# Kernel optimization log

Hardware: AMD Instinct MI355X
Metric: run time of the kernel (lower is better)

The kernel has to match this reference:

```python
import jax, jax.numpy as jnp
import numpy as np

BASE_RES = 192          # image_shape = [192, 192]
VIEWS = 128             # radial views
READOUT_OS = 2.0        # readout oversampling
SAMPLES = int(BASE_RES * READOUT_OS)  # 384 samples per spoke


def _radial_traj_and_weights():
    """Linear-ordered full-range 2D radial trajectory + ramp density weights."""
    t = jnp.arange(SAMPLES, dtype=jnp.float32)
    # radius spans [-pi, pi) along each spoke (NUFFT convention)
    r = (t - SAMPLES / 2) / (SAMPLES / 2) * jnp.pi            # [samples]
    theta = jnp.arange(VIEWS, dtype=jnp.float32) * (jnp.pi / VIEWS)  # [views]
    kx = r[None, :] * jnp.cos(theta)[:, None]                 # [views, samples]
    ky = r[None, :] * jnp.sin(theta)[:, None]
    points = jnp.stack([kx, ky], axis=-1).reshape(-1, 2)      # [M, 2]
    # geometric (ramp) density compensation: weight ~ |k| with DC floor
    rho = jnp.abs(r) / jnp.pi                                 # [samples], in [0, 1]
    w = jnp.maximum(rho, 1.0 / SAMPLES)                       # avoid zero at DC
    weights = jnp.broadcast_to(w[None, :], (VIEWS, SAMPLES)).reshape(-1)  # [M]
    return points, weights


def setup_inputs() -> dict:
    key = jax.random.key(0)
    x = jax.random.normal(key, (2, BASE_RES, BASE_RES, 2), dtype=jnp.float32)
    points, weights = _radial_traj_and_weights()
    return {"x": x, "points": points, "weights": weights}


def _nudft_resample(xc, points, weights):
    """Type-2 NUDFT (forward) -> density comp -> type-1 NUDFT (adjoint).

    xc: complex [C, B, H, W]; points: [M, 2] in [-pi, pi); weights: [M].
    The 2D nonuniform DFT phase factorizes per axis: exp(-i(kx*nx + ky*ny)).
    """
    C, B, H, W = xc.shape
    nx = (jnp.arange(H, dtype=jnp.float32) - H // 2)          # grid indices
    ny = (jnp.arange(W, dtype=jnp.float32) - W // 2)
    Ax = jnp.exp(-1j * (points[:, 0:1] * nx[None, :]).astype(jnp.complex64))  # [M, H]
    Ay = jnp.exp(-1j * (points[:, 1:2] * ny[None, :]).astype(jnp.complex64))  # [M, W]
    # type-2: k[m] = sum_{h,w} x[h,w] exp(-i(kx_m h + ky_m w))
    tmp = jnp.einsum('cbhw,mh->cbmw', xc, Ax)                 # [C, B, M, W]
    k = jnp.einsum('cbmw,mw->cbm', tmp, Ay)                   # [C, B, M]
    # density compensation
    k = k * weights.astype(jnp.complex64)
    # type-1 adjoint: img[h,w] = sum_m k[m] exp(+i(kx_m h + ky_m w))
    tmp2 = jnp.einsum('cbm,mh->cbmh', k, jnp.conj(Ax))        # [C, B, M, H]
    img = jnp.einsum('cbmh,mw->cbhw', tmp2, jnp.conj(Ay))     # [C, B, H, W]
    # scale by 1 / num_elements(image_shape)
    return img / jnp.asarray(H * W, dtype=jnp.complex64)


def reference(x, points, weights):
    # inputs [B, H, W, C] -> channels-first [C, B, H, W] (layer's perm)
    rank = x.ndim
    perm = [rank - 1] + list(range(rank - 1))
    xc = jnp.transpose(x, perm).astype(jnp.complex64)
    img = _nudft_resample(xc, points, weights)
    out = jnp.abs(img)                                        # layer dtype is real
    inv_perm = list(range(1, rank)) + [0]
    return jnp.transpose(out, inv_perm)                       # [B, H, W, C]
```

## Files before the change

kernel.cpp:

```cpp
#include <hip/hip_runtime.h>
#include <math.h>


#define HH 192
#define WW 192
#define NVIEWS 128
#define NSAMP 384
#define NPIX (HH*WW)
#define HALFT 193
#define M2 12545
#define M2P 12672
#define KTOT 25344
#define NSPLITK 33

typedef __attribute__((ext_vector_type(8))) short bf16x8;
typedef __attribute__((ext_vector_type(4))) float f32x4;
typedef __attribute__((ext_vector_type(8))) unsigned short u16x8;

__device__ __forceinline__ void rot(float& cr, float& ci, float dr, float di) {
  float nr = cr*dr - ci*di;
  float ni = cr*di + ci*dr;
  cr = nr; ci = ni;
}
__device__ __forceinline__ unsigned short f2b(float f) {
  unsigned int u = __float_as_uint(f);
  u += 0x7fffu + ((u >> 16) & 1u);
  return (unsigned short)(u >> 16);
}
__device__ __forceinline__ float b2f(unsigned short h) {
  return __uint_as_float(((unsigned int)h) << 16);
}

__global__ __launch_bounds__(256) void phase_kernel(
    const float* __restrict__ points, const float* __restrict__ x,
    unsigned short* __restrict__ BT, unsigned short* __restrict__ CxT,
    unsigned short* __restrict__ SxT, unsigned short* __restrict__ Am,
    unsigned short* __restrict__ XT, float* __restrict__ kyv) {
  const int v2 = blockIdx.x;
  const int role = blockIdx.y;
  const int t = threadIdx.x;
  if (role == 24) {
    for (int idx = v2*256 + t; idx < 768*192; idx += 65*256) {
      const int n = idx / 192, h = idx - n*192;
      const int cb = n / 192, w = n - cb*192;
      const int b = cb >> 1, c = cb & 1;
      XT[idx] = f2b(x[(((size_t)b*HH + h)*WW + w)*2 + c]);
    }
    for (int idx = v2*256 + t; idx < M2P; idx += 65*256) {
      if (idx < M2) {
        const int v2b = idx / HALFT, tb = idx - v2b*HALFT;
        kyv[idx] = points[(v2b*NSAMP + tb)*2 + 1];
      } else {
        kyv[idx] = 0.f;
      }
    }
    return;
  }
  if (t >= HALFT) return;
  if (role < 12) {
    const int hsplit = role;
    const float kx = points[(v2*NSAMP + t)*2 + 0];
    const int m2 = v2*HALFT + t;
    const int h0 = hsplit*16;
    float cr, ci; __sincosf(kx*(float)(h0-96), &ci, &cr);
    float dr, di; __sincosf(kx, &di, &dr);
    u16x8 pc, ps;
    #pragma unroll
    for (int j = 0; j < 16; ++j) {
      const int h = h0 + j;
      CxT[(size_t)h*M2P + m2] = f2b(cr);
      SxT[(size_t)h*M2P + m2] = f2b(ci);
      pc[j&7] = f2b(cr); ps[j&7] = f2b(ci);
      if ((j&7) == 7) {
        *(u16x8*)(Am + (size_t)m2*192 + (h-7))         = pc;
        *(u16x8*)(Am + (size_t)(12672+m2)*192 + (h-7)) = ps;
      }
      rot(cr, ci, dr, di);
    }
  } else {
    const int wsplit = role - 12;
    const float ky = points[(v2*NSAMP + t)*2 + 1];
    const int kap = v2*HALFT + t;
    const int w0 = wsplit*16;
    float cr, ci; __sincosf(ky*(float)(w0-96), &ci, &cr);
    float dr, di; __sincosf(ky, &di, &dr);
    #pragma unroll
    for (int j = 0; j < 16; ++j) {
      BT[(size_t)(w0+j)*KTOT + kap]       = f2b(cr);
      BT[(size_t)(w0+j)*KTOT + M2P + kap] = f2b(ci);
      rot(cr, ci, dr, di);
    }
  }
}


__global__ __launch_bounds__(256) void gemm1_kernel(
    const unsigned short* __restrict__ Am, const unsigned short* __restrict__ XT,
    const float* __restrict__ kyv, float* __restrict__ Abuf) {
  __shared__ float lds[2][128][2];
  const int L = blockIdx.x;
  const int idx0 = (L & 7)*99 + (L >> 3);
  const int mt = idx0 >> 2;
  const int cb = idx0 & 3;
  const int wv = threadIdx.x >> 6;
  const int lane = threadIdx.x & 63;
  const int r = lane & 15, kg = lane >> 4;
  const int mhalf = wv >> 1;
  const int whalf = wv & 1;
  const int mbase = mt*128 + mhalf*64;
  const int wbase = whalf*96;
  const int nbase = cb*192 + wbase;

  f32x4 acc[4][6];
  #pragma unroll
  for (int a = 0; a < 4; ++a)
    #pragma unroll
    for (int b = 0; b < 6; ++b) acc[a][b] = (f32x4){0.f,0.f,0.f,0.f};

  const unsigned short* Ap = Am + (size_t)(mbase + r)*192 + kg*8;
  const unsigned short* Bp = XT + (size_t)(nbase + r)*192 + kg*8;
  #pragma unroll
  for (int ks = 0; ks < 6; ++ks) {
    bf16x8 af[4], bfr[6];
    #pragma unroll
    for (int mf = 0; mf < 4; ++mf)
      af[mf] = *(const bf16x8*)(Ap + (size_t)mf*16*192 + ks*32);
    #pragma unroll
    for (int nf = 0; nf < 6; ++nf)
      bfr[nf] = *(const bf16x8*)(Bp + (size_t)nf*16*192 + ks*32);
    #pragma unroll
    for (int mf = 0; mf < 4; ++mf)
      #pragma unroll
      for (int nf = 0; nf < 6; ++nf)
        acc[mf][nf] = __builtin_amdgcn_mfma_f32_16x16x32_bf16(
            af[mf], bfr[nf], acc[mf][nf], 0, 0, 0);
  }

  const bool isCx = (mt < 99);
  const int m2w = mbase - (isCx ? 0 : 12672);
  float accA[16], accB[16];
  #pragma unroll
  for (int mf = 0; mf < 4; ++mf)
    #pragma unroll
    for (int reg = 0; reg < 4; ++reg) {
      const int m2 = m2w + mf*16 + kg*4 + reg;
      const float ky = kyv[m2];
      float sy, cy; __sincosf(ky*(float)(wbase + r - 96), &sy, &cy);
      float ds, dc; __sincosf(ky*16.0f, &ds, &dc);
      float a0 = 0.f, b0 = 0.f;
      #pragma unroll
      for (int nf = 0; nf < 6; ++nf) {
        const float g = acc[mf][nf][reg];
        a0 = fmaf(g, cy, a0);
        b0 = fmaf(g, sy, b0);
        rot(cy, sy, dc, ds);
      }
      accA[mf*4+reg] = a0; accB[mf*4+reg] = b0;
    }
  #pragma unroll
  for (int msk = 1; msk <= 8; msk <<= 1) {
    #pragma unroll
    for (int i = 0; i < 16; ++i) {
      accA[i] += __shfl_xor(accA[i], msk);
      accB[i] += __shfl_xor(accB[i], msk);
    }
  }
  if (r == 0) {
    #pragma unroll
    for (int mf = 0; mf < 4; ++mf)
      #pragma unroll
      for (int reg = 0; reg < 4; ++reg) {
        const int mloc = mhalf*64 + mf*16 + kg*4 + reg;
        lds[whalf][mloc][0] = accA[mf*4+reg];
        lds[whalf][mloc][1] = accB[mf*4+reg];
      }
  }
  __syncthreads();
  {
    const int tid = threadIdx.x;
    const int mloc = tid >> 1, slot = tid & 1;
    const float val = lds[0][mloc][slot] + lds[1][mloc][slot];
    const int m2 = mt*128 + mloc - (isCx ? 0 : 12672);
    const int oidx = isCx ? (slot ? 3 : 0) : (slot ? 1 : 2);
    Abuf[((size_t)cb*M2P + m2)*4 + oidx] = val;
  }
}


__global__ __launch_bounds__(256) void tmat_kernel(
    const float* __restrict__ Abuf, const float* __restrict__ weights,
    const unsigned short* __restrict__ CxT, const unsigned short* __restrict__ SxT,
    unsigned short* __restrict__ A, float* __restrict__ K2edge) {
  const int m2 = blockIdx.x*256 + threadIdx.x;
  if (m2 >= M2P) return;
  const int role = blockIdx.y;
  if (role == 192) {
    if (m2 >= M2) return;
    const int v2 = m2 / HALFT, t = m2 - v2*HALFT;
    if (t != 0 && t != 192) return;
    const float f = weights[t] * (1.0f/36864.0f);
    const bool hp = (v2 >= 1 && v2 <= 63);
    const int d = (t == 0) ? 0 : 1;
    #pragma unroll
    for (int cb = 0; cb < 4; ++cb) {
      const float4 Av = *(const float4*)(Abuf + ((size_t)cb*M2P + m2)*4);
      const float A1 = Av.x, A2 = Av.y, A3 = Av.z, A4 = Av.w;
      float* e = K2edge + ((v2*2 + d)*4 + cb)*2;
      e[0] = f*(A1 - A2); e[1] = -f*(A3 + A4);
      if (hp) {
        float* e2 = K2edge + (((128 - v2)*2 + d)*4 + cb)*2;
        e2[0] = f*(A1 + A2); e2[1] = f*(A3 - A4);
      }
    }
    return;
  }
  const int h = role;
  if (m2 >= M2) {
    #pragma unroll
    for (int cb = 0; cb < 4; ++cb) {
      unsigned short* Arow = A + (size_t)(cb*192 + h)*KTOT;
      Arow[m2] = 0; Arow[M2P + m2] = 0;
    }
    return;
  }
  const int v2 = m2 / HALFT, t = m2 - v2*HALFT;
  float f = weights[t] * (1.0f/36864.0f);
  if (t != 0 && t != 192) f *= 2.0f;
  const bool hp = (v2 >= 1 && v2 <= 63);
  const float cx = b2f(CxT[(size_t)h*M2P + m2]);
  const float sx = b2f(SxT[(size_t)h*M2P + m2]);
  #pragma unroll
  for (int cb = 0; cb < 4; ++cb) {
    const float4 Av = *(const float4*)(Abuf + ((size_t)cb*M2P + m2)*4);
    const float A1 = Av.x, A2 = Av.y, A3 = Av.z, A4 = Av.w;
    float p0, p1, q0, q1;
    if (hp) {
      p0 = 2.f*f*A1; p1 = 2.f*f*A3; q0 = 2.f*f*A4; q1 = 2.f*f*A2;
    } else {
      const float kr = f*(A1 - A2), ki = -f*(A3 + A4);
      p0 = kr; p1 = -ki; q0 = -ki; q1 = -kr;
    }
    unsigned short* Arow = A + (size_t)(cb*192 + h)*KTOT;
    Arow[m2]       = f2b(p0*cx + p1*sx);
    Arow[M2P + m2] = f2b(q0*cx + q1*sx);
  }
}

__global__ __launch_bounds__(256) void adj_gemm(
    const unsigned short* __restrict__ A, const unsigned short* __restrict__ BT,
    float* __restrict__ partials) {
  const int L = blockIdx.x;
  const int xcd = L & 7, slot = L >> 3;
  const int g = slot / 6;
  const int kc = g*8 + xcd;
  if (kc >= NSPLITK) return;
  const int mt = slot - g*6;
  const int wv = threadIdx.x >> 6;
  const int lane = threadIdx.x & 63;
  const int r = lane & 15, kg = lane >> 4;
  const int jbase = mt*128 + (wv>>1)*64;
  const int wbase = (wv&1)*96;
  const int kb = kc*768 + kg*8;

  f32x4 acc[4][6];
  #pragma unroll
  for (int a = 0; a < 4; ++a)
    #pragma unroll
    for (int b = 0; b < 6; ++b) acc[a][b] = (f32x4){0.f,0.f,0.f,0.f};

  const unsigned short* Ap = A + (size_t)(jbase + r)*KTOT + kb;
  const unsigned short* Bp = BT + (size_t)(wbase + r)*KTOT + kb;
  for (int ks = 0; ks < 24; ++ks) {
    bf16x8 af[4], bfr[6];
    #pragma unroll
    for (int mf = 0; mf < 4; ++mf)
      af[mf] = *(const bf16x8*)(Ap + (size_t)mf*16*KTOT + ks*32);
    #pragma unroll
    for (int nf = 0; nf < 6; ++nf)
      bfr[nf] = *(const bf16x8*)(Bp + (size_t)nf*16*KTOT + ks*32);
    #pragma unroll
    for (int mf = 0; mf < 4; ++mf)
      #pragma unroll
      for (int nf = 0; nf < 6; ++nf)
        acc[mf][nf] = __builtin_amdgcn_mfma_f32_16x16x32_bf16(
            af[mf], bfr[nf], acc[mf][nf], 0, 0, 0);
  }
  float* base = partials + (size_t)kc*192*768;
  #pragma unroll
  for (int mf = 0; mf < 4; ++mf)
    #pragma unroll
    for (int nf = 0; nf < 6; ++nf) {
      const int w = wbase + nf*16 + r;
      const int j = jbase + mf*16 + kg*4;
      *(f32x4*)(base + (size_t)w*768 + j) = acc[mf][nf];
    }
}

__global__ __launch_bounds__(256) void finish_kernel(
    const unsigned short* __restrict__ BT, const unsigned short* __restrict__ CxT,
    const unsigned short* __restrict__ SxT, const float* __restrict__ K2edge,
    const float* __restrict__ partials, float* __restrict__ out) {
  __shared__ float cxs[65][8], sxs[65][8], cys[65][8], sys[65][8];
  __shared__ float redI[4][64][4], redR[4][64][4];
  const int bx = blockIdx.x;
  const int h0 = (bx/24)*8, w0 = (bx%24)*8;
  const int tid = threadIdx.x;
  for (int i = tid; i < 65*8; i += 256) {
    const int v2 = i >> 3, e = i & 7;
    const int kap = v2*HALFT;
    cxs[v2][e] = b2f(CxT[(size_t)(h0+e)*M2P + kap]);
    sxs[v2][e] = b2f(SxT[(size_t)(h0+e)*M2P + kap]);
    cys[v2][e] = b2f(BT[(size_t)(w0+e)*KTOT + kap]);
    sys[v2][e] = b2f(BT[(size_t)(w0+e)*KTOT + M2P + kap]);
  }
  __syncthreads();
  const int g = tid >> 6, hi = (tid >> 3) & 7, wi = tid & 7;
  const int h = h0 + hi, w = w0 + wi;
  float im[4] = {0,0,0,0};
  for (int v = g*32; v < g*32 + 32; ++v) {
    const int v2 = (v <= 64) ? v : 128 - v;
    const float sg = (v <= 64) ? 1.f : -1.f;
    const float cx = cxs[v2][hi], sx = sg*sxs[v2][hi];
    const float cy = cys[v2][wi], sy = sys[v2][wi];
    const float t1 = cx*sy + sx*cy;
    const float t2 = cx*cy - sx*sy;
    const int idx = v*16;
    #pragma unroll
    for (int cb = 0; cb < 4; ++cb)
      im[cb] += K2edge[idx + cb*2]*t1 + K2edge[idx + cb*2 + 1]*t2;
  }
  float re[4] = {0,0,0,0};
  for (int kc = g; kc < NSPLITK; kc += 4) {
    const float* p = partials + (size_t)kc*147456 + (size_t)w*768;
    #pragma unroll
    for (int cb = 0; cb < 4; ++cb)
      re[cb] += p[cb*192 + h];
  }
  const int p = tid & 63;
  #pragma unroll
  for (int cb = 0; cb < 4; ++cb) { redI[g][p][cb] = im[cb]; redR[g][p][cb] = re[cb]; }
  __syncthreads();
  if (g == 0) {
    #pragma unroll
    for (int cb = 0; cb < 4; ++cb) {
      im[cb] += redI[1][p][cb] + redI[2][p][cb] + redI[3][p][cb];
      re[cb] += redR[1][p][cb] + redR[2][p][cb] + redR[3][p][cb];
    }
    const int pix = h*192 + w;
    #pragma unroll
    for (int b = 0; b < 2; ++b)
      #pragma unroll
      for (int c = 0; c < 2; ++c) {
        const int cb = b*2 + c;
        out[((size_t)b*NPIX + pix)*2 + c] = sqrtf(re[cb]*re[cb] + im[cb]*im[cb]);
      }
  }
}


template <int HPER>
__global__ __launch_bounds__(192) void fwd_kernel(
    const float* __restrict__ x, const float* __restrict__ points,
    float* __restrict__ kpart) {
  const int v = blockIdx.x;
  const int split = blockIdx.y;
  const int t = threadIdx.x;
  const int m = v*NSAMP + t;
  const float kx = points[2*m+0];
  const float ky = points[2*m+1];
  const int h0 = split*HPER;

  float kr[4] = {0,0,0,0}, ki[4] = {0,0,0,0};
  float cyr, cyi; __sincosf(96.0f*ky, &cyi, &cyr);
  float dyr, dyi; __sincosf(-ky, &dyi, &dyr);
  float cx0r, cx0i; __sincosf(kx*(float)(96-h0), &cx0i, &cx0r);
  float dxr, dxi; __sincosf(-kx, &dxi, &dxr);

  for (int wp = 0; wp < 96; ++wp) {
    const int w0 = wp*2;
    float g0r[4]={0,0,0,0}, g0i[4]={0,0,0,0};
    float g1r[4]={0,0,0,0}, g1i[4]={0,0,0,0};
    float cxr = cx0r, cxi = cx0i;
    const float* p0 = x + (h0*WW + w0)*2;
    const float* p1 = p0 + HH*WW*2;
    #pragma unroll 4
    for (int h = 0; h < HPER; ++h) {
      float4 a = *(const float4*)(p0 + h*(WW*2));
      float4 b = *(const float4*)(p1 + h*(WW*2));
      g0r[0] += a.x*cxr; g0i[0] += a.x*cxi;
      g0r[1] += a.y*cxr; g0i[1] += a.y*cxi;
      g1r[0] += a.z*cxr; g1i[0] += a.z*cxi;
      g1r[1] += a.w*cxr; g1i[1] += a.w*cxi;
      g0r[2] += b.x*cxr; g0i[2] += b.x*cxi;
      g0r[3] += b.y*cxr; g0i[3] += b.y*cxi;
      g1r[2] += b.z*cxr; g1i[2] += b.z*cxi;
      g1r[3] += b.w*cxr; g1i[3] += b.w*cxi;
      rot(cxr, cxi, dxr, dxi);
    }
    #pragma unroll
    for (int cb = 0; cb < 4; ++cb) {
      kr[cb] += g0r[cb]*cyr - g0i[cb]*cyi;
      ki[cb] += g0r[cb]*cyi + g0i[cb]*cyr;
    }
    rot(cyr, cyi, dyr, dyi);
    #pragma unroll
    for (int cb = 0; cb < 4; ++cb) {
      kr[cb] += g1r[cb]*cyr - g1i[cb]*cyi;
      ki[cb] += g1r[cb]*cyi + g1i[cb]*cyr;
    }
    rot(cyr, cyi, dyr, dyi);
  }
  float* o = kpart + (((split*NVIEWS + v)*192 + t)*4)*2;
  #pragma unroll
  for (int cb = 0; cb < 4; ++cb) { o[2*cb] = kr[cb]; o[2*cb+1] = ki[cb]; }
}

__global__ __launch_bounds__(256) void dc_kernel(
    const float* __restrict__ x, float* __restrict__ dcsum) {
  const int tid = threadIdx.x;
  float s0=0.f, s1=0.f, s2=0.f, s3=0.f;
  for (int i = tid; i < NPIX; i += 256) {
    float2 a = *(const float2*)(x + i*2);
    float2 b = *(const float2*)(x + HH*WW*2 + i*2);
    s0 += a.x; s1 += a.y; s2 += b.x; s3 += b.y;
  }
  #pragma unroll
  for (int off = 32; off > 0; off >>= 1) {
    s0 += __shfl_down(s0, off);
    s1 += __shfl_down(s1, off);
    s2 += __shfl_down(s2, off);
    s3 += __shfl_down(s3, off);
  }
  __shared__ float red[4][4];
  const int wv = tid >> 6, ln = tid & 63;
  if (ln == 0) { red[0][wv]=s0; red[1][wv]=s1; red[2][wv]=s2; red[3][wv]=s3; }
  __syncthreads();
  if (tid < 4) {
    float tot = red[tid][0]+red[tid][1]+red[tid][2]+red[tid][3];
    dcsum[2*tid] = tot; dcsum[2*tid+1] = 0.0f;
  }
}

__global__ __launch_bounds__(256) void combine_kernel(
    const float* __restrict__ kpart, const float* __restrict__ dcsum,
    const float* __restrict__ weights, float* __restrict__ K2, int nsplit) {
  const int idx = blockIdx.x*256 + threadIdx.x;
  if (idx >= NVIEWS*HALFT) return;
  const int v = idx / HALFT, t = idx % HALFT;
  float f = weights[t] * (1.0f/36864.0f);
  if (t != 0 && t != 192) f *= 2.0f;
  float o[8];
  if (t == 192) {
    #pragma unroll
    for (int cb = 0; cb < 4; ++cb) { o[2*cb] = f*dcsum[2*cb]; o[2*cb+1] = f*dcsum[2*cb+1]; }
  } else {
    #pragma unroll
    for (int cb = 0; cb < 4; ++cb) {
      float ar = 0.f, ai = 0.f;
      for (int s = 0; s < nsplit; ++s) {
        const float* p = kpart + (((s*NVIEWS + v)*192 + t)*4 + cb)*2;
        ar += p[0]; ai += p[1];
      }
      o[2*cb] = f*ar; o[2*cb+1] = f*ai;
    }
  }
  float* q = K2 + idx*8;
  #pragma unroll
  for (int j = 0; j < 8; ++j) q[j] = o[j];
}

template <int VPC>
__global__ __launch_bounds__(256) void adj_kernel(
    const float* __restrict__ K2, const float* __restrict__ points,
    float* __restrict__ imgpart) {
  const int pix = blockIdx.x*256 + threadIdx.x;
  const int chunk = blockIdx.y;
  const float nh = (float)(pix / WW - 96);
  const float nw = (float)(pix % WW - 96);
  float re[4] = {0,0,0,0}, im[4] = {0,0,0,0};
  const float INVPI = 0.3183098861837907f;
  const float PI192 = 3.14159265358979f / 192.0f;
  for (int v = chunk*VPC; v < chunk*VPC + VPC; ++v) {
    const float ct = -points[2*(v*NSAMP)+0] * INVPI;
    const float st = -points[2*(v*NSAMP)+1] * INVPI;
    const float alpha = ct*nh + st*nw;
    const float delta = alpha * PI192;
    float dr, di; __sincosf(delta, &di, &dr);
    float c0r, c0i; __sincosf(-192.0f*delta, &c0i, &c0r);
    const float* Kv = K2 + v*HALFT*8;
    #pragma unroll
    for (int cb = 0; cb < 4; ++cb) {
      float a = Kv[2*cb], b = Kv[2*cb+1];
      re[cb] += a*c0r - b*c0i;
      im[cb] += a*c0i + b*c0r;
    }
    float d2r = dr*dr - di*di, d2i = 2.0f*dr*di;
    float ar = c0r*dr - c0i*di, ai = c0r*di + c0i*dr;
    float br = ar*dr - ai*di,  bi = ar*di + ai*dr;
    for (int i = 0; i < 95; ++i) {
      const float* ka = Kv + (2*i+1)*8;
      const float* kb = Kv + (2*i+2)*8;
      #pragma unroll
      for (int cb = 0; cb < 4; ++cb)
        re[cb] += ka[2*cb]*ar - ka[2*cb+1]*ai;
      #pragma unroll
      for (int cb = 0; cb < 4; ++cb)
        re[cb] += kb[2*cb]*br - kb[2*cb+1]*bi;
      rot(ar, ai, d2r, d2i);
      rot(br, bi, d2r, d2i);
    }
    {
      const float* ka = Kv + 191*8;
      #pragma unroll
      for (int cb = 0; cb < 4; ++cb)
        re[cb] += ka[2*cb]*ar - ka[2*cb+1]*ai;
    }
    const float* kd = Kv + 192*8;
    #pragma unroll
    for (int cb = 0; cb < 4; ++cb) { re[cb] += kd[2*cb]; im[cb] += kd[2*cb+1]; }
  }
  float* o = imgpart + (chunk*NPIX + pix)*8;
  #pragma unroll
  for (int cb = 0; cb < 4; ++cb) { o[2*cb] = re[cb]; o[2*cb+1] = im[cb]; }
}

__global__ __launch_bounds__(256) void out_fb_kernel(
    const float* __restrict__ imgpart, float* __restrict__ out, int nchunk) {
  const int pix = blockIdx.x*256 + threadIdx.x;
  float re[4] = {0,0,0,0}, im[4] = {0,0,0,0};
  for (int ch = 0; ch < nchunk; ++ch) {
    const float* p = imgpart + (ch*NPIX + pix)*8;
    #pragma unroll
    for (int cb = 0; cb < 4; ++cb) { re[cb] += p[2*cb]; im[cb] += p[2*cb+1]; }
  }
  #pragma unroll
  for (int b = 0; b < 2; ++b)
    #pragma unroll
    for (int c = 0; c < 2; ++c) {
      const int cb = b*2 + c;
      out[(b*NPIX + pix)*2 + c] = sqrtf(re[cb]*re[cb] + im[cb]*im[cb]);
    }
}

extern "C" void kernel_launch(void* const* d_in, const int* in_sizes, int n_in,
                              void* d_out, int out_size, void* d_ws, size_t ws_size,
                              hipStream_t stream) {
  const float* x       = (const float*)d_in[0];
  const float* points  = (const float*)d_in[1];
  const float* weights = (const float*)d_in[2];
  float* out = (float*)d_out;

  const size_t OFF_S   = 20334080ull;
  const size_t SZ_AADJ = 38928384ull;
  const size_t NEED    = OFF_S + SZ_AADJ + 33ull*589824;

  if (ws_size >= NEED) {
    char* wsb = (char*)d_ws;
    unsigned short* BT   = (unsigned short*)(wsb + 0);
    unsigned short* CxT  = (unsigned short*)(wsb + 9732096);
    unsigned short* SxT  = (unsigned short*)(wsb + 14598144);
    float* K2edge        = (float*)(wsb + 19464192);
    float* kyv           = (float*)(wsb + 19472384);
    float* Abuf          = (float*)(wsb + 19523072);
    char* S              = wsb + OFF_S;
    unsigned short* Am   = (unsigned short*)(S + 0);
    unsigned short* XT   = (unsigned short*)(S + 9732096);
    unsigned short* Aadj = (unsigned short*)(S + 0);
    float* partials      = (float*)(S + SZ_AADJ);

    phase_kernel<<<dim3(65,25), 256, 0, stream>>>(points, x, BT, CxT, SxT, Am, XT, kyv);
    gemm1_kernel<<<792, 256, 0, stream>>>(Am, XT, kyv, Abuf);
    tmat_kernel<<<dim3((M2P + 255)/256, 193), 256, 0, stream>>>(
        Abuf, weights, CxT, SxT, Aadj, K2edge);
    adj_gemm<<<240, 256, 0, stream>>>(Aadj, BT, partials);
    finish_kernel<<<576, 256, 0, stream>>>(BT, CxT, SxT, K2edge, partials, out);
  } else {
    float* ws = (float*)d_ws;
    const size_t ws_floats = ws_size / sizeof(float);
    int nsplit = 16, nchunk = 16;
    auto need = [&](int ns, int nc) -> size_t {
      return (size_t)ns*196608 + 8 + 197632 + (size_t)nc*294912;
    };
    while (need(nsplit, nchunk) > ws_floats && nchunk > 1) nchunk >>= 1;
    while (need(nsplit, nchunk) > ws_floats && nsplit > 1) nsplit >>= 1;

    float* kpart   = ws;
    float* dcsum   = kpart + (size_t)nsplit*196608;
    float* K2      = dcsum + 8;
    float* imgpart = K2 + 197632;

    switch (nsplit) {
      case 16: fwd_kernel<12><<<dim3(NVIEWS,16), 192, 0, stream>>>(x, points, kpart); break;
      case 8:  fwd_kernel<24><<<dim3(NVIEWS,8),  192, 0, stream>>>(x, points, kpart); break;
      case 4:  fwd_kernel<48><<<dim3(NVIEWS,4),  192, 0, stream>>>(x, points, kpart); break;
      case 2:  fwd_kernel<96><<<dim3(NVIEWS,2),  192, 0, stream>>>(x, points, kpart); break;
      default: fwd_kernel<192><<<dim3(NVIEWS,1), 192, 0, stream>>>(x, points, kpart); break;
    }
    dc_kernel<<<1, 256, 0, stream>>>(x, dcsum);
    combine_kernel<<<(NVIEWS*HALFT + 255)/256, 256, 0, stream>>>(
        kpart, dcsum, weights, K2, nsplit);
    switch (nchunk) {
      case 16: adj_kernel<8>  <<<dim3(NPIX/256,16), 256, 0, stream>>>(K2, points, imgpart); break;
      case 8:  adj_kernel<16> <<<dim3(NPIX/256,8),  256, 0, stream>>>(K2, points, imgpart); break;
      case 4:  adj_kernel<32> <<<dim3(NPIX/256,4),  256, 0, stream>>>(K2, points, imgpart); break;
      case 2:  adj_kernel<64> <<<dim3(NPIX/256,2),  256, 0, stream>>>(K2, points, imgpart); break;
      default: adj_kernel<128><<<dim3(NPIX/256,1),  256, 0, stream>>>(K2, points, imgpart); break;
    }
    out_fb_kernel<<<NPIX/256, 256, 0, stream>>>(imgpart, out, nchunk);
  }
}
```

Before: 125.1 us.

## Fuse adjoint A-matrix construction into adj_gemm operand loads

The tmat kernel used to materialize a large bf16 A matrix (768 rows by 25344 columns) that adj_gemm then read back. Now a small combine kernel writes 16 per-sample coefficient rows, and adj_gemm builds each A fragment on the fly from those coefficients and the CxT/SxT phase tables before the MFMA. This removes roughly 39 MB of write plus read traffic and one large launch. The cost is extra global loads and ALU conversion work inside the GEMM inner loop, repeated across column tiles.

Result: slower. 144.3 us (+15.3%).

```diff
diff --git a/kernel.cpp b/kernel.cpp
--- a/kernel.cpp
+++ b/kernel.cpp
@@ -186,53 +186,24 @@
   }
 }
 
-
-__global__ __launch_bounds__(256) void tmat_kernel(
+__global__ __launch_bounds__(256) void combine2_kernel(
     const float* __restrict__ Abuf, const float* __restrict__ weights,
-    const unsigned short* __restrict__ CxT, const unsigned short* __restrict__ SxT,
-    unsigned short* __restrict__ A, float* __restrict__ K2edge) {
+    float* __restrict__ combos, float* __restrict__ K2edge) {
   const int m2 = blockIdx.x*256 + threadIdx.x;
   if (m2 >= M2P) return;
-  const int role = blockIdx.y;
-  if (role == 192) {
-    if (m2 >= M2) return;
-    const int v2 = m2 / HALFT, t = m2 - v2*HALFT;
-    if (t != 0 && t != 192) return;
-    const float f = weights[t] * (1.0f/36864.0f);
-    const bool hp = (v2 >= 1 && v2 <= 63);
-    const int d = (t == 0) ? 0 : 1;
-    #pragma unroll
-    for (int cb = 0; cb < 4; ++cb) {
-      const float4 Av = *(const float4*)(Abuf + ((size_t)cb*M2P + m2)*4);
-      const float A1 = Av.x, A2 = Av.y, A3 = Av.z, A4 = Av.w;
-      float* e = K2edge + ((v2*2 + d)*4 + cb)*2;
-      e[0] = f*(A1 - A2); e[1] = -f*(A3 + A4);
-      if (hp) {
-        float* e2 = K2edge + (((128 - v2)*2 + d)*4 + cb)*2;
-        e2[0] = f*(A1 + A2); e2[1] = f*(A3 - A4);
-      }
-    }
-    return;
-  }
-  const int h = role;
   if (m2 >= M2) {
     #pragma unroll
-    for (int cb = 0; cb < 4; ++cb) {
-      unsigned short* Arow = A + (size_t)(cb*192 + h)*KTOT;
-      Arow[m2] = 0; Arow[M2P + m2] = 0;
-    }
+    for (int q = 0; q < 16; ++q) combos[(size_t)q*M2P + m2] = 0.f;
     return;
   }
   const int v2 = m2 / HALFT, t = m2 - v2*HALFT;
   float f = weights[t] * (1.0f/36864.0f);
   if (t != 0 && t != 192) f *= 2.0f;
   const bool hp = (v2 >= 1 && v2 <= 63);
-  const float cx = b2f(CxT[(size_t)h*M2P + m2]);
-  const float sx = b2f(SxT[(size_t)h*M2P + m2]);
   #pragma unroll
   for (int cb = 0; cb < 4; ++cb) {
-    const float4 Av = *(const float4*)(Abuf + ((size_t)cb*M2P + m2)*4);
-    const float A1 = Av.x, A2 = Av.y, A3 = Av.z, A4 = Av.w;
+    const float4 A = *(const float4*)(Abuf + ((size_t)cb*M2P + m2)*4);
+    const float A1 = A.x, A2 = A.y, A3 = A.z, A4 = A.w;
     float p0, p1, q0, q1;
     if (hp) {
       p0 = 2.f*f*A1; p1 = 2.f*f*A3; q0 = 2.f*f*A4; q1 = 2.f*f*A2;
@@ -240,14 +211,26 @@
       const float kr = f*(A1 - A2), ki = -f*(A3 + A4);
       p0 = kr; p1 = -ki; q0 = -ki; q1 = -kr;
     }
-    unsigned short* Arow = A + (size_t)(cb*192 + h)*KTOT;
-    Arow[m2]       = f2b(p0*cx + p1*sx);
-    Arow[M2P + m2] = f2b(q0*cx + q1*sx);
+    combos[(size_t)(cb*4+0)*M2P + m2] = p0;
+    combos[(size_t)(cb*4+1)*M2P + m2] = p1;
+    combos[(size_t)(cb*4+2)*M2P + m2] = q0;
+    combos[(size_t)(cb*4+3)*M2P + m2] = q1;
+    if (t == 0 || t == 192) {
+      const int d = (t == 0) ? 0 : 1;
+      const float fe = weights[t] * (1.0f/36864.0f);
+      float* e = K2edge + ((v2*2 + d)*4 + cb)*2;
+      e[0] = fe*(A1 - A2); e[1] = -fe*(A3 + A4);
+      if (hp) {
+        float* e2 = K2edge + (((128 - v2)*2 + d)*4 + cb)*2;
+        e2[0] = fe*(A1 + A2); e2[1] = fe*(A3 - A4);
+      }
+    }
   }
 }
 
 __global__ __launch_bounds__(256) void adj_gemm(
-    const unsigned short* __restrict__ A, const unsigned short* __restrict__ BT,
+    const float* __restrict__ combos, const unsigned short* __restrict__ CxT,
+    const unsigned short* __restrict__ SxT, const unsigned short* __restrict__ BT,
     float* __restrict__ partials) {
   const int L = blockIdx.x;
   const int xcd = L & 7, slot = L >> 3;
@@ -268,22 +251,41 @@
     #pragma unroll
     for (int b = 0; b < 6; ++b) acc[a][b] = (f32x4){0.f,0.f,0.f,0.f};
 
-  const unsigned short* Ap = A + (size_t)(jbase + r)*KTOT + kb;
   const unsigned short* Bp = BT + (size_t)(wbase + r)*KTOT + kb;
   for (int ks = 0; ks < 24; ++ks) {
-    bf16x8 af[4], bfr[6];
-    #pragma unroll
-    for (int mf = 0; mf < 4; ++mf)
-      af[mf] = *(const bf16x8*)(Ap + (size_t)mf*16*KTOT + ks*32);
+    bf16x8 bfr[6];
     #pragma unroll
     for (int nf = 0; nf < 6; ++nf)
       bfr[nf] = *(const bf16x8*)(Bp + (size_t)nf*16*KTOT + ks*32);
-    #pragma unroll
-    for (int mf = 0; mf < 4; ++mf)
+
+    const int kap = kb + ks*32;
+    const bool isQ = (kap >= M2P);
+    const int m2c = kap - (isQ ? M2P : 0);
+    const int off = isQ ? 2 : 0;
+
+    #pragma unroll
+    for (int mf = 0; mf < 4; ++mf) {
+      const int j = jbase + mf*16 + r;
+      const int cb = j / 192;
+      const int h  = j - cb*192;
+      const u16x8 cxv = *(const u16x8*)(CxT + (size_t)h*M2P + m2c);
+      const u16x8 sxv = *(const u16x8*)(SxT + (size_t)h*M2P + m2c);
+      const float* crow = combos + (size_t)(cb*4 + off)*M2P + m2c;
+      float pc[8], ps[8];
+      *(float4*)&pc[0] = *(const float4*)(crow);
+      *(float4*)&pc[4] = *(const float4*)(crow + 4);
+      *(float4*)&ps[0] = *(const float4*)(crow + M2P);
+      *(float4*)&ps[4] = *(const float4*)(crow + M2P + 4);
+      u16x8 av;
+      #pragma unroll
+      for (int e = 0; e < 8; ++e)
+        av[e] = f2b(pc[e]*b2f(cxv[e]) + ps[e]*b2f(sxv[e]));
+      const bf16x8 af = *(const bf16x8*)&av;
       #pragma unroll
       for (int nf = 0; nf < 6; ++nf)
         acc[mf][nf] = __builtin_amdgcn_mfma_f32_16x16x32_bf16(
-            af[mf], bfr[nf], acc[mf][nf], 0, 0, 0);
+            af, bfr[nf], acc[mf][nf], 0, 0, 0);
+    }
   }
   float* base = partials + (size_t)kc*192*768;
   #pragma unroll
@@ -550,9 +552,8 @@
   const float* weights = (const float*)d_in[2];
   float* out = (float*)d_out;
 
-  const size_t OFF_S   = 20334080ull;
-  const size_t SZ_AADJ = 38928384ull;
-  const size_t NEED    = OFF_S + SZ_AADJ + 33ull*589824;
+  const size_t OFF_S = 21145088ull;
+  const size_t NEED  = OFF_S + 19464192ull;
 
   if (ws_size >= NEED) {
     char* wsb = (char*)d_ws;
@@ -562,17 +563,17 @@
     float* K2edge        = (float*)(wsb + 19464192);
     float* kyv           = (float*)(wsb + 19472384);
     float* Abuf          = (float*)(wsb + 19523072);
+    float* combos        = (float*)(wsb + 20334080);
     char* S              = wsb + OFF_S;
     unsigned short* Am   = (unsigned short*)(S + 0);
     unsigned short* XT   = (unsigned short*)(S + 9732096);
-    unsigned short* Aadj = (unsigned short*)(S + 0);
-    float* partials      = (float*)(S + SZ_AADJ);
+    float* partials      = (float*)(S + 0);
 
     phase_kernel<<<dim3(65,25), 256, 0, stream>>>(points, x, BT, CxT, SxT, Am, XT, kyv);
     gemm1_kernel<<<792, 256, 0, stream>>>(Am, XT, kyv, Abuf);
-    tmat_kernel<<<dim3((M2P + 255)/256, 193), 256, 0, stream>>>(
-        Abuf, weights, CxT, SxT, Aadj, K2edge);
-    adj_gemm<<<240, 256, 0, stream>>>(Aadj, BT, partials);
+    combine2_kernel<<<(M2P + 255)/256, 256, 0, stream>>>(
+        Abuf, weights, combos, K2edge);
+    adj_gemm<<<240, 256, 0, stream>>>(combos, CxT, SxT, BT, partials);
     finish_kernel<<<576, 256, 0, stream>>>(BT, CxT, SxT, K2edge, partials, out);
   } else {
     float* ws = (float*)d_ws;
```
